# Kernel tuning notes

Measured on AMD Instinct MI355X. Metric: run time of the kernel, lower is better.

Reference implementation:

```python
import jax, jax.numpy as jnp
import numpy as np

N_GRAPHS = 128
N_NODES = 512
N = N_GRAPHS * N_NODES      # 65536 total nodes
E = 524288                  # edges (avg degree 8)
F_IN = 4                    # num_features
EMB = 4                     # embedding_dim
HEADS = 4
GDIM = 16                   # GATConv_dim
D = GDIM * HEADS            # 64 = d_model
NHEAD = 2                   # heads // 2
FF = 64                     # ff_hid_dim
OUT = 64                    # output_dim
N_GAT_REST = 3              # gat_layers - 1


def setup_inputs() -> dict:
    key = jax.random.key(0)
    ks = iter(jax.random.split(key, 64))
    def nrm(shape, fan_in):
        return jax.random.normal(next(ks), shape, jnp.float32) / np.float32(np.sqrt(fan_in))
    inp = {}
    inp['x'] = jax.random.normal(next(ks), (N, F_IN), jnp.float32)
    inp['edge_index'] = jax.random.randint(next(ks), (2, E), 0, N, dtype=jnp.int32)
    inp['batch'] = jnp.repeat(jnp.arange(N_GRAPHS, dtype=jnp.int32), N_NODES)
    # feature_fc
    inp['Wf'] = nrm((F_IN, EMB), F_IN); inp['bf'] = jnp.zeros((EMB,), jnp.float32)
    # input GATConv (EMB -> HEADS*GDIM)
    inp['gW0'] = nrm((EMB, HEADS * GDIM), EMB)
    inp['aS0'] = nrm((HEADS, GDIM), GDIM); inp['aD0'] = nrm((HEADS, GDIM), GDIM)
    inp['gb0'] = jnp.zeros((D,), jnp.float32)
    # remaining 3 GATConv layers (D -> HEADS*GDIM), stacked
    inp['gW'] = nrm((N_GAT_REST, D, HEADS * GDIM), D)
    inp['aS'] = nrm((N_GAT_REST, HEADS, GDIM), GDIM); inp['aD'] = nrm((N_GAT_REST, HEADS, GDIM), GDIM)
    inp['gb'] = jnp.zeros((N_GAT_REST, D), jnp.float32)
    # decoder layer: self-attn, cross-attn, layernorms, FFN
    for p in ['sWq','sWk','sWv','sWo','cWq','cWk','cWv','cWo']:
        inp[p] = nrm((D, D), D)
    for p in ['sbq','sbk','sbv','sbo','cbq','cbk','cbv','cbo']:
        inp[p] = jnp.zeros((D,), jnp.float32)
    for g, b in [('ln1g','ln1b'), ('ln2g','ln2b'), ('ln3g','ln3b')]:
        inp[g] = jnp.ones((D,), jnp.float32); inp[b] = jnp.zeros((D,), jnp.float32)
    inp['ffW1'] = nrm((D, FF), D); inp['ffb1'] = jnp.zeros((FF,), jnp.float32)
    inp['ffW2'] = nrm((FF, D), FF); inp['ffb2'] = jnp.zeros((D,), jnp.float32)
    inp['fcW'] = nrm((D, OUT), D); inp['fcb'] = jnp.zeros((OUT,), jnp.float32)
    return inp


def _gat(h_in, src, dst, W, a_s, a_d, b):
    # PyG GATConv, concat=True, negative_slope=0.2, self-loops already in (src,dst)
    h = (h_in @ W).reshape(N, HEADS, GDIM)
    es = jnp.einsum('nho,ho->nh', h, a_s)   # [N,H]
    ed = jnp.einsum('nho,ho->nh', h, a_d)
    e = jax.nn.leaky_relu(es[src] + ed[dst], 0.2)          # [E',H]
    m = jax.ops.segment_max(e, dst, num_segments=N)        # segment softmax over dst
    w = jnp.exp(e - m[dst])
    s = jax.ops.segment_sum(w, dst, num_segments=N)
    alpha = w / (s[dst] + 1e-16)
    out = jax.ops.segment_sum(h[src] * alpha[..., None], dst, num_segments=N)
    return out.reshape(N, D) + b


def _mha(q, kv, Wq, bq, Wk, bk, Wv, bv, Wo, bo):
    B, S, Dm = q.shape
    hd = Dm // NHEAD
    Q = (q @ Wq + bq).reshape(B, S, NHEAD, hd)
    K = (kv @ Wk + bk).reshape(B, S, NHEAD, hd)
    V = (kv @ Wv + bv).reshape(B, S, NHEAD, hd)
    a = jax.nn.softmax(jnp.einsum('bqhd,bkhd->bhqk', Q, K) / jnp.sqrt(jnp.float32(hd)), axis=-1)
    o = jnp.einsum('bhqk,bkhd->bqhd', a, V).reshape(B, S, Dm)
    return o @ Wo + bo


def _ln(x, g, b):
    m = x.mean(-1, keepdims=True)
    v = ((x - m) ** 2).mean(-1, keepdims=True)
    return (x - m) / jnp.sqrt(v + 1e-5) * g + b


def reference(x, edge_index, batch, Wf, bf, gW0, aS0, aD0, gb0, gW, aS, aD, gb,
              sWq, sWk, sWv, sWo, cWq, cWk, cWv, cWo,
              sbq, sbk, sbv, sbo, cbq, cbk, cbv, cbo,
              ln1g, ln1b, ln2g, ln2b, ln3g, ln3b,
              ffW1, ffb1, ffW2, ffb2, fcW, fcb):
    loops = jnp.arange(N, dtype=edge_index.dtype)
    src = jnp.concatenate([edge_index[0], loops])
    dst = jnp.concatenate([edge_index[1], loops])
    h = x @ Wf + bf
    h = jax.nn.leaky_relu(_gat(h, src, dst, gW0, aS0, aD0, gb0), 0.01)
    for i in range(N_GAT_REST):
        h = jax.nn.leaky_relu(_gat(h, src, dst, gW[i], aS[i], aD[i], gb[i]), 0.01)
    t = h.reshape(N_GRAPHS, N_NODES, D)
    # one transformer decoder layer, post-norm, memory = layer input
    mem = t
    t = _ln(t + _mha(t, t, sWq, sbq, sWk, sbk, sWv, sbv, sWo, sbo), ln1g, ln1b)
    t = _ln(t + _mha(t, mem, cWq, cbq, cWk, cbk, cWv, cbv, cWo, cbo), ln2g, ln2b)
    t = _ln(t + (jax.nn.relu(t @ ffW1 + ffb1) @ ffW2 + ffb2), ln3g, ln3b)
    h = t.reshape(N, D)
    pooled = jax.ops.segment_sum(h, batch, num_segments=N_GRAPHS) / jnp.float32(N_NODES)
    return pooled @ fcW + fcb
```

## Files before the change

### kernel.cpp

```cpp
#include <hip/hip_runtime.h>
#include <math.h>

#define NG 128
#define SEQ 512
#define NN 65536
#define EE 524288
#define DM 64
#define HSTR 80

typedef __attribute__((ext_vector_type(8))) short short8;
typedef __attribute__((ext_vector_type(4))) short short4v;
typedef __attribute__((ext_vector_type(4))) float f32x4;

__device__ __forceinline__ float lrelu(float x, float s){ return x > 0.f ? x : s*x; }

__device__ __forceinline__ unsigned short f2bf(float x){
  union { float f; unsigned u; } v; v.f = x;
  unsigned r = v.u + 0x7FFF + ((v.u>>16)&1);
  return (unsigned short)(r>>16);
}
__device__ __forceinline__ float bf2f(unsigned short x){
  union { unsigned u; float f; } v; v.u = ((unsigned)x)<<16;
  return v.f;
}
// ... 78 lines not shown
    float s = 0.f;
    #pragma unroll
    for (int k=0;k<4;k++) s += Wf[i*4+k]*gW0[k*64+j];
    Wl[i][j] = s;
  }
  if (tid < 64){
    float4 v = *(const float4*)&x[(size_t)(n0+tid)*4];
    inL[0][tid]=v.x; inL[1][tid]=v.y; inL[2][tid]=v.z; inL[3][tid]=v.w;
  }
  __syncthreads();
  int i = tid>>4, j = tid&15;
  float acc[4][4];
  #pragma unroll
  for (int r=0;r<4;r++){
    #pragma unroll
    for (int c=0;c<4;c++) acc[r][c] = 0.f;
  }
  #pragma unroll
  for (int k=0;k<4;k++){
    float4 av = *(float4*)&inL[k][4*i];
    float4 bv = *(float4*)&Wl[k][4*j];
    float a_[4]={av.x,av.y,av.z,av.w}, b_[4]={bv.x,bv.y,bv.z,bv.w};
    #pragma unroll
    for (int r=0;r<4;r++){
      #pragma unroll
      for (int c=0;c<4;c++) acc[r][c] += a_[r]*b_[c];
    }
  }
  float4 asv = *(float4*)&asl[4*j];
  float4 adv = *(float4*)&adl[4*j];
  float4 bbv = *(float4*)&b0l[4*j];
  float bb[4] = {bbv.x, bbv.y, bbv.z, bbv.w};
  #pragma unroll
  for (int r=0;r<4;r++){
    float y0=acc[r][0]+bb[0], y1=acc[r][1]+bb[1], y2=acc[r][2]+bb[2], y3=acc[r][3]+bb[3];
    int node = n0 + 4*i + r;
    ushort4 hv;
    hv.x=f2bf(y0); hv.y=f2bf(y1); hv.z=f2bf(y2); hv.w=f2bf(y3);
    *(ushort4*)&hout[(size_t)node*HSTR + 4*j] = hv;
    float ps = y0*asv.x + y1*asv.y + y2*asv.z + y3*asv.w;
    float pd = y0*adv.x + y1*adv.y + y2*adv.z + y3*adv.w;
    ps += __shfl_xor(ps,1); ps += __shfl_xor(ps,2);
    pd += __shfl_xor(pd,1); pd += __shfl_xor(pd,2);
    if ((j&3)==0){
      *(float*)&hout[(size_t)node*HSTR + 64 + 2*(j>>2)] = ps;
      ed[(size_t)node*4 + (j>>2)] = pd;
    }
  }
}

__global__ void __launch_bounds__(256) k_transform_bf(const unsigned short* __restrict__ hin, const float* __restrict__ W,
                            const float* __restrict__ aSp, const float* __restrict__ aDp,
                            unsigned short* __restrict__ hout, float* __restrict__ ed){
  __shared__ float inL[64][68];
  __shared__ float Wl[64][64];
  __shared__ float asl[64], adl[64];
  int tid = threadIdx.x;
  int n0 = blockIdx.x*64;
  if (tid < 64){ asl[tid] = aSp[tid]; adl[tid] = aDp[tid]; }
  for (int idx=tid; idx<1024; idx+=256){
    int k = idx>>4, jj = (idx&15)<<2;
    *(float4*)&Wl[k][jj] = *(const float4*)&W[k*64+jj];
  }
  for (int idx=tid; idx<1024; idx+=256){
    int node = idx>>4, kk = (idx&15)<<2;
    ushort4 v = *(const ushort4*)&hin[(size_t)(n0+node)*64 + kk];
    inL[kk][node]=bf2f(v.x); inL[kk+1][node]=bf2f(v.y); inL[kk+2][node]=bf2f(v.z); inL[kk+3][node]=bf2f(v.w);
  }
  __syncthreads();
  int i = tid>>4, j = tid&15;
  float acc[4][4];
  #pragma unroll
  for (int r=0;r<4;r++){
    #pragma unroll
    for (int c=0;c<4;c++) acc[r][c] = 0.f;
  }
  #pragma unroll 4
  for (int k=0;k<64;k++){
    float4 av = *(float4*)&inL[k][4*i];
    float4 bv = *(float4*)&Wl[k][4*j];
    float a_[4]={av.x,av.y,av.z,av.w}, b_[4]={bv.x,bv.y,bv.z,bv.w};
    #pragma unroll
    for (int r=0;r<4;r++){
      #pragma unroll
      for (int c=0;c<4;c++) acc[r][c] += a_[r]*b_[c];
    }
  }
  float4 asv = *(float4*)&asl[4*j];
  float4 adv = *(float4*)&adl[4*j];
  #pragma unroll
  for (int r=0;r<4;r++){
    float y0=acc[r][0], y1=acc[r][1], y2=acc[r][2], y3=acc[r][3];
    int node = n0 + 4*i + r;
    ushort4 hv;
    hv.x=f2bf(y0); hv.y=f2bf(y1); hv.z=f2bf(y2); hv.w=f2bf(y3);
    *(ushort4*)&hout[(size_t)node*HSTR + 4*j] = hv;
    float ps = y0*asv.x + y1*asv.y + y2*asv.z + y3*asv.w;
    float pd = y0*adv.x + y1*adv.y + y2*adv.z + y3*adv.w;
    ps += __shfl_xor(ps,1); ps += __shfl_xor(ps,2);
    pd += __shfl_xor(pd,1); pd += __shfl_xor(pd,2);
    if ((j&3)==0){
      *(float*)&hout[(size_t)node*HSTR + 64 + 2*(j>>2)] = ps;
      ed[(size_t)node*4 + (j>>2)] = pd;
    }
  }
}

template<int BF16OUT>
__global__ void __launch_bounds__(256) k_aggregate(const unsigned short* __restrict__ h,
                            const float* __restrict__ ed, const int* __restrict__ rowp,
                            const int* __restrict__ col, const float* __restrict__ gb,
                            void* __restrict__ houtv){
  int tid = threadIdx.x;
  int n = blockIdx.x*4 + (tid>>6);
  int l = tid&63;
  int q = l>>4;
  int sl = l&15;
  int head = sl>>2;
  float edn = ed[(size_t)n*4 + head];
  float es_self = *(const float*)&h[(size_t)n*HSTR + 64 + 2*head];
  int beg = __builtin_amdgcn_readfirstlane(rowp[n]);
  int end = __builtin_amdgcn_readfirstlane(rowp[n+1]);
  float m = -1e30f, s = 0.f;
  float a0=0.f, a1=0.f, a2=0.f, a3=0.f;
  int i = beg;
  for (; i+8 <= end; i += 8){
    int c0=col[i], c1=col[i+1], c2=col[i+2], c3=col[i+3];
    int c4=col[i+4], c5=col[i+5], c6=col[i+6], c7=col[i+7];
    int t01 = (q&1)? c1 : c0;
    int t23 = (q&1)? c3 : c2;
    int sq0 = (q&2)? t23 : t01;
    int t45 = (q&1)? c5 : c4;
    int t67 = (q&1)? c7 : c6;
    int sq1 = (q&2)? t67 : t45;
    size_t b0r = (size_t)sq0*HSTR, b1r = (size_t)sq1*HSTR;
    ushort4 hv0 = *(const ushort4*)&h[b0r + 4*sl];
    ushort4 hv1 = *(const ushort4*)&h[b1r + 4*sl];
    float e0 = lrelu(*(const float*)&h[b0r + 64 + 2*head] + edn, 0.2f);
    float e1 = lrelu(*(const float*)&h[b1r + 64 + 2*head] + edn, 0.2f);
    float mx = fmaxf(e0, e1);
    if (__any(mx > m + 8.f)){
      float nm = fmaxf(m, mx);
      float c = __expf(m - nm);
      s*=c; a0*=c; a1*=c; a2*=c; a3*=c; m = nm;
    }
    float w0 = __expf(e0 - m);
    float w1 = __expf(e1 - m);
    s += w0 + w1;
    a0 += w0*bf2f(hv0.x) + w1*bf2f(hv1.x);
    a1 += w0*bf2f(hv0.y) + w1*bf2f(hv1.y);
    a2 += w0*bf2f(hv0.z) + w1*bf2f(hv1.z);
    a3 += w0*bf2f(hv0.w) + w1*bf2f(hv1.w);
  }
  if (i < end){
    int last = end-1;
    int i1=(i+1<last)?i+1:last, i2=(i+2<last)?i+2:last, i3=(i+3<last)?i+3:last;
    int i4=(i+4<last)?i+4:last, i5=(i+5<last)?i+5:last, i6=(i+6<last)?i+6:last;
    int c0=col[i], c1=col[i1], c2=col[i2], c3=col[i3];
    int c4=col[i4], c5=col[i5], c6=col[i6], c7=col[last];
    int t01 = (q&1)? c1 : c0;
    int t23 = (q&1)? c3 : c2;
    int sq0 = (q&2)? t23 : t01;
    int t45 = (q&1)? c5 : c4;
    int t67 = (q&1)? c7 : c6;
    int sq1 = (q&2)? t67 : t45;
// ... 5 lines not shown
    float e0 = lrelu(*(const float*)&h[b0r + 64 + 2*head] + edn, 0.2f);
    float e1 = lrelu(*(const float*)&h[b1r + 64 + 2*head] + edn, 0.2f);
    if (!ac0) e0 = -1e30f;
    if (!ac1) e1 = -1e30f;
    float mx = fmaxf(e0, e1);
    if (__any(mx > m + 8.f)){
      float nm = fmaxf(m, mx);
      float c = __expf(m - nm);
      s*=c; a0*=c; a1*=c; a2*=c; a3*=c; m = nm;
    }
    float w0 = ac0 ? __expf(e0 - m) : 0.f;
    float w1 = ac1 ? __expf(e1 - m) : 0.f;
    s += w0 + w1;
    a0 += w0*bf2f(hv0.x) + w1*bf2f(hv1.x);
    a1 += w0*bf2f(hv0.y) + w1*bf2f(hv1.y);
    a2 += w0*bf2f(hv0.z) + w1*bf2f(hv1.z);
    a3 += w0*bf2f(hv0.w) + w1*bf2f(hv1.w);
  }
  #pragma unroll
  for (int off=16; off<=32; off<<=1){
    float m2 = __shfl_xor(m, off);
    float s2 = __shfl_xor(s, off);
    float b0 = __shfl_xor(a0, off);
    float b1 = __shfl_xor(a1, off);
    float b2 = __shfl_xor(a2, off);
    float b3 = __shfl_xor(a3, off);
    float nm = fmaxf(m, m2);
    float c1 = __expf(m - nm), c2 = __expf(m2 - nm);
    s  = s*c1  + s2*c2;
    a0 = a0*c1 + b0*c2;
    a1 = a1*c1 + b1*c2;
    a2 = a2*c1 + b2*c2;
    a3 = a3*c1 + b3*c2;
    m = nm;
  }
  {
    float e_self = lrelu(es_self + edn, 0.2f);
    float nm = fmaxf(m, e_self);
    float c = __expf(m - nm), cs = __expf(e_self - nm);
    ushort4 hs = *(const ushort4*)&h[(size_t)n*HSTR + 4*sl];
    s  = s*c  + cs;
    a0 = a0*c + cs*bf2f(hs.x);
    a1 = a1*c + cs*bf2f(hs.y);
    a2 = a2*c + cs*bf2f(hs.z);
    a3 = a3*c + cs*bf2f(hs.w);
  }
  if (q == 0){
    float inv = 1.f/(s + 1e-16f);
    float4 gv = *(const float4*)&gb[4*sl];
    float o0 = lrelu(a0*inv + gv.x, 0.01f);
    float o1 = lrelu(a1*inv + gv.y, 0.01f);
    float o2 = lrelu(a2*inv + gv.z, 0.01f);
    float o3 = lrelu(a3*inv + gv.w, 0.01f);
    if (BF16OUT){
      ushort4 hv; hv.x=f2bf(o0); hv.y=f2bf(o1); hv.z=f2bf(o2); hv.w=f2bf(o3);
      *(ushort4*)((unsigned short*)houtv + (size_t)n*64 + 4*sl) = hv;
    } else {
      *(float4*)((float*)houtv + (size_t)n*64 + 4*sl) = make_float4(o0,o1,o2,o3);
    }
  }
}

__global__ void __launch_bounds__(256) k_qkv3(const float* __restrict__ in0, const float* __restrict__ W0, const float* __restrict__ b0, unsigned short* __restrict__ o0,
                      const float* __restrict__ in1, const float* __restrict__ W1, const float* __restrict__ b1, unsigned short* __restrict__ o1,
                      const float* __restrict__ in2, const float* __restrict__ W2, const float* __restrict__ b2, unsigned short* __restrict__ o2,
                      float scl0){
  __shared__ float inL[64][68];
  __shared__ float Wl[64][64];
  int tid = threadIdx.x;
  int n0 = blockIdx.x*64;
  int i = tid>>4, j = tid&15;
  const float* ins[3] = {in0, in1, in2};
  const float* Ws[3] = {W0, W1, W2};
  const float* bs[3] = {b0, b1, b2};
  unsigned short* os[3] = {o0, o1, o2};
  const float* cur = nullptr;
  for (int w=0; w<3; w++){
    __syncthreads();
    if (ins[w] != cur){
      cur = ins[w];
      for (int idx=tid; idx<1024; idx+=256){
        int node = idx>>4, kk = (idx&15)<<2;
        float4 v = *(const float4*)&cur[(size_t)(n0+node)*64 + kk];
        inL[kk][node]=v.x; inL[kk+1][node]=v.y; inL[kk+2][node]=v.z; inL[kk+3][node]=v.w;
      }
    }
    for (int idx=tid; idx<1024; idx+=256){
      int k = idx>>4, jj = (idx&15)<<2;
      *(float4*)&Wl[k][jj] = *(const float4*)&Ws[w][k*64+jj];
    }
    __syncthreads();
    float acc[4][4];
    #pragma unroll
    for (int r=0;r<4;r++){
      #pragma unroll
      for (int c=0;c<4;c++) acc[r][c] = 0.f;
    }
    #pragma unroll 4
    for (int k=0;k<64;k++){
      float4 av = *(float4*)&inL[k][4*i];
      float4 bv = *(float4*)&Wl[k][4*j];
      float a_[4]={av.x,av.y,av.z,av.w}, b_[4]={bv.x,bv.y,bv.z,bv.w};
      #pragma unroll
      for (int r=0;r<4;r++){
        #pragma unroll
        for (int c=0;c<4;c++) acc[r][c] += a_[r]*b_[c];
      }
    }
    float4 bv = *(const float4*)&bs[w][4*j];
    float bb[4] = {bv.x, bv.y, bv.z, bv.w};
    float sc = (w==0) ? scl0 : 1.f;
    #pragma unroll
    for (int r=0;r<4;r++){
      ushort4 hv;
      hv.x = f2bf((acc[r][0]+bb[0])*sc);
      hv.y = f2bf((acc[r][1]+bb[1])*sc);
      hv.z = f2bf((acc[r][2]+bb[2])*sc);
      hv.w = f2bf((acc[r][3]+bb[3])*sc);
      *(ushort4*)&os[w][(size_t)(n0+4*i+r)*64 + 4*j] = hv;
    }
  }
}

__global__ void __launch_bounds__(256) k_ffn(const float* __restrict__ in,
                     const float* __restrict__ W1p, const float* __restrict__ b1p,
                     const float* __restrict__ W2p, const float* __restrict__ b2p,
                     const float* __restrict__ g, const float* __restrict__ bl,
                     float* __restrict__ out){
  __shared__ float inL[64][68];
  __shared__ float Wl[64][64];
  __shared__ float ffL[64][68];
  int tid = threadIdx.x;
  int n0 = blockIdx.x*64;
  for (int idx=tid; idx<1024; idx+=256){
    int k = idx>>4, jj = (idx&15)<<2;
    *(float4*)&Wl[k][jj] = *(const float4*)&W1p[k*64+jj];
  }
  for (int idx=tid; idx<1024; idx+=256){
    int node = idx>>4, kk = (idx&15)<<2;
    float4 v = *(const float4*)&in[(size_t)(n0+node)*64 + kk];
    inL[kk][node]=v.x; inL[kk+1][node]=v.y; inL[kk+2][node]=v.z; inL[kk+3][node]=v.w;
  }
  __syncthreads();
  int i = tid>>4, j = tid&15;
  float acc[4][4];
  #pragma unroll
  for (int r=0;r<4;r++){
    #pragma unroll
    for (int c=0;c<4;c++) acc[r][c] = 0.f;
  }
  #pragma unroll 4
  for (int k=0;k<64;k++){
    float4 av = *(float4*)&inL[k][4*i];
    float4 bv = *(float4*)&Wl[k][4*j];
    float a_[4]={av.x,av.y,av.z,av.w}, b_[4]={bv.x,bv.y,bv.z,bv.w};
    #pragma unroll
    for (int r=0;r<4;r++){
      #pragma unroll
      for (int c=0;c<4;c++) acc[r][c] += a_[r]*b_[c];
    }
  }
  float4 b1v = *(const float4*)&b1p[4*j];
  float bb1[4] = {b1v.x, b1v.y, b1v.z, b1v.w};
  #pragma unroll
  for (int r=0;r<4;r++){
    #pragma unroll
    for (int c=0;c<4;c++){
      ffL[4*j+c][4*i+r] = fmaxf(acc[r][c] + bb1[c], 0.f);
    }
  }
  __syncthreads();
  for (int idx=tid; idx<1024; idx+=256){
    int k = idx>>4, jj = (idx&15)<<2;
    *(float4*)&Wl[k][jj] = *(const float4*)&W2p[k*64+jj];
  }
  __syncthreads();
  #pragma unroll
  for (int r=0;r<4;r++){
    #pragma unroll
    for (int c=0;c<4;c++) acc[r][c] = 0.f;
  }
  #pragma unroll 4
  for (int k=0;k<64;k++){
    float4 av = *(float4*)&ffL[k][4*i];
    float4 bv = *(float4*)&Wl[k][4*j];
    float a_[4]={av.x,av.y,av.z,av.w}, b_[4]={bv.x,bv.y,bv.z,bv.w};
    #pragma unroll
    for (int r=0;r<4;r++){
      #pragma unroll
      for (int c=0;c<4;c++) acc[r][c] += a_[r]*b_[c];
    }
  }
  float4 b2v = *(const float4*)&b2p[4*j];
  float bb2v[4] = {b2v.x, b2v.y, b2v.z, b2v.w};
  float4 gv = *(const float4*)&g[4*j];
  float4 blv = *(const float4*)&bl[4*j];
  float gg[4] = {gv.x, gv.y, gv.z, gv.w};
  float bbl[4] = {blv.x, blv.y, blv.z, blv.w};
  #pragma unroll
  for (int r=0;r<4;r++){
    int node = n0 + 4*i + r;
    float y[4];
    #pragma unroll
    for (int c=0;c<4;c++) y[c] = acc[r][c] + bb2v[c] + inL[4*j+c][4*i+r];
    float s = (y[0]+y[1]) + (y[2]+y[3]);
    s += __shfl_xor(s,1); s += __shfl_xor(s,2); s += __shfl_xor(s,4); s += __shfl_xor(s,8);
    float mean = s * (1.f/64.f);
    float d[4] = {y[0]-mean, y[1]-mean, y[2]-mean, y[3]-mean};
    float v = (d[0]*d[0]+d[1]*d[1]) + (d[2]*d[2]+d[3]*d[3]);
    v += __shfl_xor(v,1); v += __shfl_xor(v,2); v += __shfl_xor(v,4); v += __shfl_xor(v,8);
    float inv = rsqrtf(v*(1.f/64.f) + 1e-5f);
    *(float4*)&out[(size_t)node*64 + 4*j] =
      make_float4(d[0]*inv*gg[0]+bbl[0], d[1]*inv*gg[1]+bbl[1],
                  d[2]*inv*gg[2]+bbl[2], d[3]*inv*gg[3]+bbl[3]);
  }
}

__global__ void __launch_bounds__(512) k_attn_fused(const unsigned short* __restrict__ Q, const unsigned short* __restrict__ K,
                      const unsigned short* __restrict__ V,
                      const float* __restrict__ Wo, const float* __restrict__ bo,
                      const float* __restrict__ res, const float* __restrict__ g, const float* __restrict__ bl,
                      float* __restrict__ out){
  __shared__ __align__(16) char smem[49152];
  char* Ksm = smem;
  char* Vsm = smem + 16384;
  char* Psm = smem + 32768;

  int bid = blockIdx.x;
  int qq = bid & 3;
  int b  = bid >> 2;
  int tid = threadIdx.x;
  int wave = tid>>6;
  int l = tid & 63;
  int lq = l & 15;
  int g4 = l >> 4;
  int head = wave & 1;
  int qg = wave >> 1;
  const size_t gb = (size_t)b*SEQ*64;
  const int hoff = head*32;
  const f32x4 zero = {0.f,0.f,0.f,0.f};

  int qrow0 = qq*128 + qg*32;
  short8 qf[2];
  f32x4 O[2][2];
  float m_[2], l_[2];
  #pragma unroll
  for (int qt=0; qt<2; qt++){
    qf[qt] = *(const short8*)(Q + gb + (size_t)(qrow0 + qt*16 + lq)*64 + hoff + g4*8);
    O[qt][0] = zero; O[qt][1] = zero;
    m_[qt] = -1e30f; l_[qt] = 0.f;
  }
  char* Pw = Psm + wave*2048;
  int swzp = (lq&7)<<4;
  int d0 = hoff + lq, d1 = hoff + lq + 16;
  int sv0 = (((d0&7) ^ ((d0>>3)&7)) << 4);
  int sv1 = (((d1&7) ^ ((d1>>3)&7)) << 4);

  for (int ph=0; ph<4; ph++){
    __syncthreads();
    #pragma unroll
    for (int it=0; it<2; it++){
      int idx = tid + it*512;
      int row = idx>>3, gr = idx&7;
      uint4 v = *(const uint4*)(K + gb + (size_t)(ph*128 + row)*64 + gr*8);
      *(uint4*)(Ksm + row*128 + ((gr*16) ^ ((row&7)<<4))) = v;
    }
    #pragma unroll
    for (int it=0; it<2; it++){
      int idx = tid + it*512;
      int key = idx>>3, gr = idx&7;
      uint4 vv = *(const uint4*)(V + gb + (size_t)(ph*128 + key)*64 + gr*8);
      const unsigned short* vs = (const unsigned short*)&vv;
      #pragma unroll
      for (int c=0;c<8;c++){
        int d = gr*8 + c;
// ... 73 lines not shown
    lt += __shfl_xor(lt, 32);
    float inv = 1.f/lt;
    int row = qg*32 + qt*16 + lq;
    #pragma unroll
    for (int c=0;c<4;c++){
      OT[(hoff + g4*4 + c)*136 + row]      = f2bf(O[qt][0][c]*inv);
      OT[(hoff + 16 + g4*4 + c)*136 + row] = f2bf(O[qt][1][c]*inv);
    }
  }
  for (int idx=tid; idx<1024; idx+=512){
    int k = idx>>4, jj = (idx&15)<<2;
    *(float4*)&WoL[k*64+jj] = *(const float4*)&Wo[k*64+jj];
  }
  __syncthreads();
  int i = tid>>4, j = tid&15;
  float acc[4][4];
  #pragma unroll
  for (int r=0;r<4;r++){
    #pragma unroll
    for (int c=0;c<4;c++) acc[r][c] = 0.f;
  }
  #pragma unroll 4
  for (int k=0;k<64;k++){
    short4v av = *(short4v*)&OT[k*136 + 4*i];
    float4 bv = *(float4*)&WoL[k*64 + 4*j];
    float b_[4]={bv.x,bv.y,bv.z,bv.w};
    #pragma unroll
    for (int r=0;r<4;r++){
      float a = bf2f((unsigned short)av[r]);
      #pragma unroll
      for (int c=0;c<4;c++) acc[r][c] += a*b_[c];
    }
  }
  float4 bov = *(const float4*)&bo[4*j];
  float4 gv = *(const float4*)&g[4*j];
  float4 blv = *(const float4*)&bl[4*j];
  float bb[4] = {bov.x, bov.y, bov.z, bov.w};
  float gg[4] = {gv.x, gv.y, gv.z, gv.w};
  float bbl[4] = {blv.x, blv.y, blv.z, blv.w};
  #pragma unroll
  for (int r=0;r<4;r++){
    int row = 4*i + r;
    int node = b*SEQ + qq*128 + row;
    float4 rv = *(const float4*)&res[(size_t)node*64 + 4*j];
    float y[4] = {acc[r][0]+bb[0]+rv.x, acc[r][1]+bb[1]+rv.y,
                  acc[r][2]+bb[2]+rv.z, acc[r][3]+bb[3]+rv.w};
    float s = (y[0]+y[1]) + (y[2]+y[3]);
    s += __shfl_xor(s,1); s += __shfl_xor(s,2); s += __shfl_xor(s,4); s += __shfl_xor(s,8);
    float mean = s * (1.f/64.f);
    float d[4] = {y[0]-mean, y[1]-mean, y[2]-mean, y[3]-mean};
    float v = (d[0]*d[0]+d[1]*d[1]) + (d[2]*d[2]+d[3]*d[3]);
    v += __shfl_xor(v,1); v += __shfl_xor(v,2); v += __shfl_xor(v,4); v += __shfl_xor(v,8);
    float inv = rsqrtf(v*(1.f/64.f) + 1e-5f);
    *(float4*)&out[(size_t)node*64 + 4*j] =
      make_float4(d[0]*inv*gg[0]+bbl[0], d[1]*inv*gg[1]+bbl[1],
                  d[2]*inv*gg[2]+bbl[2], d[3]*inv*gg[3]+bbl[3]);
  }
}

__global__ void __launch_bounds__(256) k_pool_fc(const float* __restrict__ t, const float* __restrict__ fcW,
                          const float* __restrict__ fcb, float* __restrict__ out){
  __shared__ float pl[4][64];
  __shared__ float pf[64];
  int b = blockIdx.x;
  int tid = threadIdx.x;
  int j = tid&63, seg = tid>>6;
  const float* basep = t + (size_t)b*SEQ*64;
  float s = 0.f;
  for (int si=seg*128; si<(seg+1)*128; si++) s += basep[(size_t)si*64 + j];
  pl[seg][j] = s;
  __syncthreads();
  if (tid < 64){
    pf[tid] = (pl[0][tid]+pl[1][tid]+pl[2][tid]+pl[3][tid]) * (1.f/512.f);
  }
  __syncthreads();
  if (tid < 64){
    float o = fcb[tid];
    for (int k=0;k<64;k++) o += pf[k]*fcW[k*64+tid];
    out[(size_t)b*64 + tid] = o;
  }
}

extern "C" void kernel_launch(void* const* d_in, const int* in_sizes, int n_in,
                              void* d_out, int out_size, void* d_ws, size_t ws_size,
                              hipStream_t stream) {
  const float* x    = (const float*)d_in[0];
  const int*   ei   = (const int*)d_in[1];
  const float* Wf   = (const float*)d_in[3];
  const float* bf   = (const float*)d_in[4];
  const float* gW0  = (const float*)d_in[5];
  const float* aS0  = (const float*)d_in[6];
  const float* aD0  = (const float*)d_in[7];
  const float* gb0  = (const float*)d_in[8];
  const float* gW   = (const float*)d_in[9];
  const float* aS   = (const float*)d_in[10];
  const float* aD   = (const float*)d_in[11];
  const float* gb   = (const float*)d_in[12];
  const float* sWq  = (const float*)d_in[13];
  const float* sWk  = (const float*)d_in[14];
  const float* sWv  = (const float*)d_in[15];
  const float* sWo  = (const float*)d_in[16];
  const float* cWq  = (const float*)d_in[17];
  const float* cWk  = (const float*)d_in[18];
  const float* cWv  = (const float*)d_in[19];
  const float* cWo  = (const float*)d_in[20];
  const float* sbq  = (const float*)d_in[21];
  const float* sbk  = (const float*)d_in[22];
  const float* sbv  = (const float*)d_in[23];
  const float* sbo  = (const float*)d_in[24];
  const float* cbq  = (const float*)d_in[25];
  const float* cbk  = (const float*)d_in[26];
  const float* cbv  = (const float*)d_in[27];
  const float* cbo  = (const float*)d_in[28];
  const float* ln1g = (const float*)d_in[29];
  const float* ln1b = (const float*)d_in[30];
  const float* ln2g = (const float*)d_in[31];
  const float* ln2b = (const float*)d_in[32];
  const float* ln3g = (const float*)d_in[33];
  const float* ln3b = (const float*)d_in[34];
  const float* ffW1 = (const float*)d_in[35];
  const float* ffb1 = (const float*)d_in[36];
  const float* ffW2 = (const float*)d_in[37];
  const float* ffb2 = (const float*)d_in[38];
  const float* fcW  = (const float*)d_in[39];
  const float* fcb  = (const float*)d_in[40];

  char* ws = (char*)d_ws;
  size_t off = 0;
  auto alloc = [&](size_t bytes) -> void* {
    void* p = ws + off;
    off += (bytes + 255) & ~(size_t)255;
    return p;
  };
  int* deg    = (int*)alloc(NN*sizeof(int));
  int* excl   = (int*)alloc(NN*sizeof(int));
  int* rowp   = (int*)alloc((NN+1)*sizeof(int));
  int* cursor = (int*)alloc(NN*sizeof(int));
  int* col    = (int*)alloc(EE*sizeof(int));
  int* bsums  = (int*)alloc(256*sizeof(int));
  float* ed   = (float*)alloc((size_t)NN*4*sizeof(float));
  unsigned short* Hb   = (unsigned short*)alloc((size_t)NN*HSTR*sizeof(unsigned short));
  unsigned short* Hagg = (unsigned short*)alloc((size_t)NN*64*sizeof(unsigned short));
  unsigned short* Qb = (unsigned short*)alloc((size_t)NN*64*sizeof(unsigned short));
  unsigned short* Kb = (unsigned short*)alloc((size_t)NN*64*sizeof(unsigned short));
  unsigned short* Vb = (unsigned short*)alloc((size_t)NN*64*sizeof(unsigned short));
  float* B1   = (float*)alloc((size_t)NN*64*sizeof(float));
  float* B2   = (float*)alloc((size_t)NN*64*sizeof(float));
  float* B5   = (float*)alloc((size_t)NN*64*sizeof(float));

  const int* e_src = ei;
  const int* e_dst = ei + EE;

  const float scale = 0.17677669529663687f;

  hipMemsetAsync(deg, 0, NN*sizeof(int), stream);
  k_count<<<EE/256, 256, 0, stream>>>(e_dst, deg);
  k_scan1<<<NN/256, 256, 0, stream>>>(deg, excl, bsums);
  k_scan2<<<1, 256, 0, stream>>>(bsums);
  k_scan3<<<NN/256, 256, 0, stream>>>(excl, bsums, rowp, cursor);
  k_fill<<<EE/256, 256, 0, stream>>>(e_src, e_dst, cursor, col);

  k_transform0<<<NN/64, 256, 0, stream>>>(x, Wf, bf, gW0, aS0, aD0, Hb, ed);
  k_aggregate<1><<<NN/4, 256, 0, stream>>>(Hb, ed, rowp, col, gb0, Hagg);
  k_transform_bf<<<NN/64, 256, 0, stream>>>(Hagg, gW+0*4096, aS+0*64, aD+0*64, Hb, ed);
  k_aggregate<1><<<NN/4, 256, 0, stream>>>(Hb, ed, rowp, col, gb+0*64, Hagg);
  k_transform_bf<<<NN/64, 256, 0, stream>>>(Hagg, gW+1*4096, aS+1*64, aD+1*64, Hb, ed);
  k_aggregate<1><<<NN/4, 256, 0, stream>>>(Hb, ed, rowp, col, gb+1*64, Hagg);
  k_transform_bf<<<NN/64, 256, 0, stream>>>(Hagg, gW+2*4096, aS+2*64, aD+2*64, Hb, ed);
  k_aggregate<0><<<NN/4, 256, 0, stream>>>(Hb, ed, rowp, col, gb+2*64, B2);

  k_qkv3<<<NN/64, 256, 0, stream>>>(B2, sWq, sbq, Qb, B2, sWk, sbk, Kb, B2, sWv, sbv, Vb, scale);
  k_attn_fused<<<NG*4, 512, 0, stream>>>(Qb, Kb, Vb, sWo, sbo, B2, ln1g, ln1b, B5);

  k_qkv3<<<NN/64, 256, 0, stream>>>(B5, cWq, cbq, Qb, B2, cWk, cbk, Kb, B2, cWv, cbv, Vb, scale);
  k_attn_fused<<<NG*4, 512, 0, stream>>>(Qb, Kb, Vb, cWo, cbo, B5, ln2g, ln2b, B2);

  k_ffn<<<NN/64, 256, 0, stream>>>(B2, ffW1, ffb1, ffW2, ffb2, ln3g, ln3b, B1);

  k_pool_fc<<<NG, 256, 0, stream>>>(B1, fcW, fcb, (float*)d_out);
}
```

Before: 409.0 us.

## Use bf16 MFMA for dense node transforms, QKV projections and FFN

Replaces the scalar FP32 register-tiled 64x64 GEMMs in the GAT transform, QKV projection and FFN kernels with bf16 MFMA 16x16x32 instructions, staging inputs and transposed weights in swizzled LDS. To feed these, the aggregate and attention kernels now also write bf16 copies of their outputs, so the GEMM kernels read half-width activations. The FP32 residual path is kept for the layernorms. This cuts ALU work and input bandwidth in the GEMM kernels, at the cost of extra bf16 stores and reduced precision in the QKV and FFN inputs.

```diff
diff --git a/kernel.cpp b/kernel.cpp
--- a/kernel.cpp
+++ b/kernel.cpp
@@ -154,65 +154,76 @@
 __global__ void __launch_bounds__(256) k_transform_bf(const unsigned short* __restrict__ hin, const float* __restrict__ W,
                             const float* __restrict__ aSp, const float* __restrict__ aDp,
                             unsigned short* __restrict__ hout, float* __restrict__ ed){
-  __shared__ float inL[64][68];
-  __shared__ float Wl[64][64];
+  __shared__ __align__(16) char Ab[8192];
+  __shared__ __align__(16) char Wt[8192];
   __shared__ float asl[64], adl[64];
   int tid = threadIdx.x;
   int n0 = blockIdx.x*64;
-  if (tid < 64){ asl[tid] = aSp[tid]; adl[tid] = aDp[tid]; }
-  for (int idx=tid; idx<1024; idx+=256){
-    int k = idx>>4, jj = (idx&15)<<2;
-    *(float4*)&Wl[k][jj] = *(const float4*)&W[k*64+jj];
-  }
-  for (int idx=tid; idx<1024; idx+=256){
-    int node = idx>>4, kk = (idx&15)<<2;
-    ushort4 v = *(const ushort4*)&hin[(size_t)(n0+node)*64 + kk];
-    inL[kk][node]=bf2f(v.x); inL[kk+1][node]=bf2f(v.y); inL[kk+2][node]=bf2f(v.z); inL[kk+3][node]=bf2f(v.w);
-  }
-  __syncthreads();
-  int i = tid>>4, j = tid&15;
-  float acc[4][4];
-  #pragma unroll
-  for (int r=0;r<4;r++){
-    #pragma unroll
-    for (int c=0;c<4;c++) acc[r][c] = 0.f;
-  }
-  #pragma unroll 4
-  for (int k=0;k<64;k++){
-    float4 av = *(float4*)&inL[k][4*i];
-    float4 bv = *(float4*)&Wl[k][4*j];
-    float a_[4]={av.x,av.y,av.z,av.w}, b_[4]={bv.x,bv.y,bv.z,bv.w};
+  if (tid < 64){ asl[tid]=aSp[tid]; adl[tid]=aDp[tid]; }
+  #pragma unroll
+  for (int it=0; it<2; it++){
+    int idx = tid + it*256;
+    int row = idx>>3, gr = idx&7;
+    uint4 v = *(const uint4*)(hin + (size_t)(n0+row)*64 + gr*8);
+    *(uint4*)(Ab + row*128 + ((gr*16) ^ ((row&7)<<4))) = v;
+  }
+  #pragma unroll
+  for (int it=0; it<4; it++){
+    int idx = tid + it*256;
+    int k = idx>>4, c4 = (idx&15)<<2;
+    float4 v = *(const float4*)(W + k*64 + c4);
+    float vv[4]={v.x,v.y,v.z,v.w};
+    #pragma unroll
+    for (int c=0;c<4;c++){
+      int col = c4+c;
+      *(unsigned short*)(Wt + col*128 + ((2*k) ^ ((col&7)<<4))) = f2bf(vv[c]);
+    }
+  }
+  __syncthreads();
+  int wave = tid>>6, l=tid&63, lq=l&15, g4=l>>4;
+  int nb = wave*16;
+  const f32x4 zero = {0.f,0.f,0.f,0.f};
+  short8 af[2];
+  #pragma unroll
+  for (int s=0;s<2;s++){
+    int row = nb+lq;
+    af[s] = *(short8*)(Ab + row*128 + (((s*64)+g4*16) ^ ((row&7)<<4)));
+  }
+  f32x4 acc[4];
+  #pragma unroll
+  for (int ct=0;ct<4;ct++){
+    acc[ct]=zero;
+    #pragma unroll
+    for (int s=0;s<2;s++){
+      int col = ct*16+lq;
+      short8 wf = *(short8*)(Wt + col*128 + (((s*64)+g4*16) ^ ((col&7)<<4)));
+      acc[ct] = __builtin_amdgcn_mfma_f32_16x16x32_bf16(af[s], wf, acc[ct], 0,0,0);
+    }
+  }
+  #pragma unroll
+  for (int ct=0;ct<4;ct++){
+    float as_ = asl[ct*16+lq], ad_ = adl[ct*16+lq];
     #pragma unroll
     for (int r=0;r<4;r++){
-      #pragma unroll
-      for (int c=0;c<4;c++) acc[r][c] += a_[r]*b_[c];
-    }
-  }
-  float4 asv = *(float4*)&asl[4*j];
-  float4 adv = *(float4*)&adl[4*j];
-  #pragma unroll
-  for (int r=0;r<4;r++){
-    float y0=acc[r][0], y1=acc[r][1], y2=acc[r][2], y3=acc[r][3];
-    int node = n0 + 4*i + r;
-    ushort4 hv;
-    hv.x=f2bf(y0); hv.y=f2bf(y1); hv.z=f2bf(y2); hv.w=f2bf(y3);
-    *(ushort4*)&hout[(size_t)node*HSTR + 4*j] = hv;
-    float ps = y0*asv.x + y1*asv.y + y2*asv.z + y3*asv.w;
-    float pd = y0*adv.x + y1*adv.y + y2*adv.z + y3*adv.w;
-    ps += __shfl_xor(ps,1); ps += __shfl_xor(ps,2);
-    pd += __shfl_xor(pd,1); pd += __shfl_xor(pd,2);
-    if ((j&3)==0){
-      *(float*)&hout[(size_t)node*HSTR + 64 + 2*(j>>2)] = ps;
-      ed[(size_t)node*4 + (j>>2)] = pd;
-    }
-  }
-}
-
-template<int BF16OUT>
+      float y = acc[ct][r];
+      int node = n0 + nb + 4*g4 + r;
+      hout[(size_t)node*HSTR + ct*16 + lq] = f2bf(y);
+      float ps = y*as_, pd = y*ad_;
+      ps += __shfl_xor(ps,1); ps += __shfl_xor(ps,2); ps += __shfl_xor(ps,4); ps += __shfl_xor(ps,8);
+      pd += __shfl_xor(pd,1); pd += __shfl_xor(pd,2); pd += __shfl_xor(pd,4); pd += __shfl_xor(pd,8);
+      if (lq==0){
+        *(float*)&hout[(size_t)node*HSTR + 64 + 2*ct] = ps;
+        ed[(size_t)node*4 + ct] = pd;
+      }
+    }
+  }
+}
+
+template<int MODE>
 __global__ void __launch_bounds__(256) k_aggregate(const unsigned short* __restrict__ h,
                             const float* __restrict__ ed, const int* __restrict__ rowp,
                             const int* __restrict__ col, const float* __restrict__ gb,
-                            void* __restrict__ houtv){
+                            float* __restrict__ fout, unsigned short* __restrict__ bout){
   int tid = threadIdx.x;
   int n = blockIdx.x*4 + (tid>>6);
   int l = tid&63;
@@ -324,167 +335,196 @@
     float o1 = lrelu(a1*inv + gv.y, 0.01f);
     float o2 = lrelu(a2*inv + gv.z, 0.01f);
     float o3 = lrelu(a3*inv + gv.w, 0.01f);
-    if (BF16OUT){
+    if (MODE==0 || MODE==2){
+      *(float4*)(fout + (size_t)n*64 + 4*sl) = make_float4(o0,o1,o2,o3);
+    }
+    if (MODE==1 || MODE==2){
       ushort4 hv; hv.x=f2bf(o0); hv.y=f2bf(o1); hv.z=f2bf(o2); hv.w=f2bf(o3);
-      *(ushort4*)((unsigned short*)houtv + (size_t)n*64 + 4*sl) = hv;
-    } else {
-      *(float4*)((float*)houtv + (size_t)n*64 + 4*sl) = make_float4(o0,o1,o2,o3);
-    }
-  }
-}
-
-__global__ void __launch_bounds__(256) k_qkv3(const float* __restrict__ in0, const float* __restrict__ W0, const float* __restrict__ b0, unsigned short* __restrict__ o0,
-                      const float* __restrict__ in1, const float* __restrict__ W1, const float* __restrict__ b1, unsigned short* __restrict__ o1,
-                      const float* __restrict__ in2, const float* __restrict__ W2, const float* __restrict__ b2, unsigned short* __restrict__ o2,
+      *(ushort4*)(bout + (size_t)n*64 + 4*sl) = hv;
+    }
+  }
+}
+
+__global__ void __launch_bounds__(256) k_qkv3(const unsigned short* __restrict__ in0, const float* __restrict__ W0, const float* __restrict__ b0, unsigned short* __restrict__ o0,
+                      const unsigned short* __restrict__ in1, const float* __restrict__ W1, const float* __restrict__ b1, unsigned short* __restrict__ o1,
+                      const unsigned short* __restrict__ in2, const float* __restrict__ W2, const float* __restrict__ b2, unsigned short* __restrict__ o2,
                       float scl0){
-  __shared__ float inL[64][68];
-  __shared__ float Wl[64][64];
+  __shared__ __align__(16) char Ab[8192];
+  __shared__ __align__(16) char Wt[8192];
   int tid = threadIdx.x;
   int n0 = blockIdx.x*64;
-  int i = tid>>4, j = tid&15;
-  const float* ins[3] = {in0, in1, in2};
+  int wave = tid>>6, l=tid&63, lq=l&15, g4=l>>4;
+  int nb = wave*16;
+  const f32x4 zero = {0.f,0.f,0.f,0.f};
+  const unsigned short* ins[3] = {in0, in1, in2};
   const float* Ws[3] = {W0, W1, W2};
   const float* bs[3] = {b0, b1, b2};
   unsigned short* os[3] = {o0, o1, o2};
-  const float* cur = nullptr;
+  const unsigned short* cur = nullptr;
+  short8 af[2];
   for (int w=0; w<3; w++){
+    bool restage = (ins[w] != cur);
     __syncthreads();
-    if (ins[w] != cur){
+    if (restage){
       cur = ins[w];
-      for (int idx=tid; idx<1024; idx+=256){
-        int node = idx>>4, kk = (idx&15)<<2;
-        float4 v = *(const float4*)&cur[(size_t)(n0+node)*64 + kk];
-        inL[kk][node]=v.x; inL[kk+1][node]=v.y; inL[kk+2][node]=v.z; inL[kk+3][node]=v.w;
+      #pragma unroll
+      for (int it=0; it<2; it++){
+        int idx = tid + it*256;
+        int row = idx>>3, gr = idx&7;
+        uint4 v = *(const uint4*)(cur + (size_t)(n0+row)*64 + gr*8);
+        *(uint4*)(Ab + row*128 + ((gr*16) ^ ((row&7)<<4))) = v;
       }
     }
-    for (int idx=tid; idx<1024; idx+=256){
-      int k = idx>>4, jj = (idx&15)<<2;
-      *(float4*)&Wl[k][jj] = *(const float4*)&Ws[w][k*64+jj];
+    #pragma unroll
+    for (int it=0; it<4; it++){
+      int idx = tid + it*256;
+      int k = idx>>4, c4 = (idx&15)<<2;
+      float4 v = *(const float4*)(Ws[w] + k*64 + c4);
+      float vv[4]={v.x,v.y,v.z,v.w};
+      #pragma unroll
+      for (int c=0;c<4;c++){
+        int colc = c4+c;
+        *(unsigned short*)(Wt + colc*128 + ((2*k) ^ ((colc&7)<<4))) = f2bf(vv[c]);
+      }
     }
     __syncthreads();
-    float acc[4][4];
-    #pragma unroll
-    for (int r=0;r<4;r++){
+    if (restage){
       #pragma unroll
-      for (int c=0;c<4;c++) acc[r][c] = 0.f;
-    }
-    #pragma unroll 4
-    for (int k=0;k<64;k++){
-      float4 av = *(float4*)&inL[k][4*i];
-      float4 bv = *(float4*)&Wl[k][4*j];
-      float a_[4]={av.x,av.y,av.z,av.w}, b_[4]={bv.x,bv.y,bv.z,bv.w};
+      for (int s=0;s<2;s++){
+        int row = nb+lq;
+        af[s] = *(short8*)(Ab + row*128 + (((s*64)+g4*16) ^ ((row&7)<<4)));
+      }
+    }
+    float sc = (w==0) ? scl0 : 1.f;
+    #pragma unroll
+    for (int ct=0;ct<4;ct++){
+      f32x4 acc = zero;
+      #pragma unroll
+      for (int s=0;s<2;s++){
+        int colc = ct*16+lq;
+        short8 wf = *(short8*)(Wt + colc*128 + (((s*64)+g4*16) ^ ((colc&7)<<4)));
+        acc = __builtin_amdgcn_mfma_f32_16x16x32_bf16(af[s], wf, acc, 0,0,0);
+      }
+      float bv = bs[w][ct*16+lq];
       #pragma unroll
       for (int r=0;r<4;r++){
-        #pragma unroll
-        for (int c=0;c<4;c++) acc[r][c] += a_[r]*b_[c];
+        int node = n0 + nb + 4*g4 + r;
+        os[w][(size_t)node*64 + ct*16 + lq] = f2bf((acc[r] + bv)*sc);
       }
     }
-    float4 bv = *(const float4*)&bs[w][4*j];
-    float bb[4] = {bv.x, bv.y, bv.z, bv.w};
-    float sc = (w==0) ? scl0 : 1.f;
-    #pragma unroll
-    for (int r=0;r<4;r++){
-      ushort4 hv;
-      hv.x = f2bf((acc[r][0]+bb[0])*sc);
-      hv.y = f2bf((acc[r][1]+bb[1])*sc);
-      hv.z = f2bf((acc[r][2]+bb[2])*sc);
-      hv.w = f2bf((acc[r][3]+bb[3])*sc);
-      *(ushort4*)&os[w][(size_t)(n0+4*i+r)*64 + 4*j] = hv;
-    }
-  }
-}
-
-__global__ void __launch_bounds__(256) k_ffn(const float* __restrict__ in,
+  }
+}
+
+__global__ void __launch_bounds__(256) k_ffn(const unsigned short* __restrict__ inb, const float* __restrict__ inf,
                      const float* __restrict__ W1p, const float* __restrict__ b1p,
                      const float* __restrict__ W2p, const float* __restrict__ b2p,
                      const float* __restrict__ g, const float* __restrict__ bl,
                      float* __restrict__ out){
-  __shared__ float inL[64][68];
-  __shared__ float Wl[64][64];
-  __shared__ float ffL[64][68];
+  __shared__ __align__(16) char Ab[8192];
+  __shared__ __align__(16) char Wt[8192];
   int tid = threadIdx.x;
   int n0 = blockIdx.x*64;
-  for (int idx=tid; idx<1024; idx+=256){
-    int k = idx>>4, jj = (idx&15)<<2;
-    *(float4*)&Wl[k][jj] = *(const float4*)&W1p[k*64+jj];
-  }
-  for (int idx=tid; idx<1024; idx+=256){
-    int node = idx>>4, kk = (idx&15)<<2;
-    float4 v = *(const float4*)&in[(size_t)(n0+node)*64 + kk];
-    inL[kk][node]=v.x; inL[kk+1][node]=v.y; inL[kk+2][node]=v.z; inL[kk+3][node]=v.w;
-  }
-  __syncthreads();
-  int i = tid>>4, j = tid&15;
-  float acc[4][4];
+  int wave = tid>>6, l=tid&63, lq=l&15, g4=l>>4;
+  int nb = wave*16;
+  const f32x4 zero = {0.f,0.f,0.f,0.f};
+  #pragma unroll
+  for (int it=0; it<2; it++){
+    int idx = tid + it*256;
+    int row = idx>>3, gr = idx&7;
+    uint4 v = *(const uint4*)(inb + (size_t)(n0+row)*64 + gr*8);
+    *(uint4*)(Ab + row*128 + ((gr*16) ^ ((row&7)<<4))) = v;
+  }
+  #pragma unroll
+  for (int it=0; it<4; it++){
+    int idx = tid + it*256;
+    int k = idx>>4, c4 = (idx&15)<<2;
+    float4 v = *(const float4*)(W1p + k*64 + c4);
+    float vv[4]={v.x,v.y,v.z,v.w};
+    #pragma unroll
+    for (int c=0;c<4;c++){
+      int colc = c4+c;
+      *(unsigned short*)(Wt + colc*128 + ((2*k) ^ ((colc&7)<<4))) = f2bf(vv[c]);
+    }
+  }
+  __syncthreads();
+  short8 af[2];
+  #pragma unroll
+  for (int s=0;s<2;s++){
+    int row = nb+lq;
+    af[s] = *(short8*)(Ab + row*128 + (((s*64)+g4*16) ^ ((row&7)<<4)));
+  }
+  #pragma unroll
+  for (int ct=0;ct<4;ct++){
+    f32x4 acc = zero;
+    #pragma unroll
+    for (int s=0;s<2;s++){
+      int colc = ct*16+lq;
+      short8 wf = *(short8*)(Wt + colc*128 + (((s*64)+g4*16) ^ ((colc&7)<<4)));
+      acc = __builtin_amdgcn_mfma_f32_16x16x32_bf16(af[s], wf, acc, 0,0,0);
+    }
+    float bv = b1p[ct*16+lq];
+    #pragma unroll
+    for (int r=0;r<4;r++){
+      int row = nb + 4*g4 + r;
+      float y = fmaxf(acc[r] + bv, 0.f);
+      *(unsigned short*)(Ab + row*128 + ((2*(ct*16+lq)) ^ ((row&7)<<4))) = f2bf(y);
+    }
+  }
+  __syncthreads();
+  #pragma unroll
+  for (int it=0; it<4; it++){
+    int idx = tid + it*256;
+    int k = idx>>4, c4 = (idx&15)<<2;
+    float4 v = *(const float4*)(W2p + k*64 + c4);
+    float vv[4]={v.x,v.y,v.z,v.w};
+    #pragma unroll
+    for (int c=0;c<4;c++){
+      int colc = c4+c;
+      *(unsigned short*)(Wt + colc*128 + ((2*k) ^ ((colc&7)<<4))) = f2bf(vv[c]);
+    }
+  }
+  __syncthreads();
+  #pragma unroll
+  for (int s=0;s<2;s++){
+    int row = nb+lq;
+    af[s] = *(short8*)(Ab + row*128 + (((s*64)+g4*16) ^ ((row&7)<<4)));
+  }
+  float yv[4][4];
+  #pragma unroll
+  for (int ct=0;ct<4;ct++){
+    f32x4 acc = zero;
+    #pragma unroll
+    for (int s=0;s<2;s++){
+      int colc = ct*16+lq;
+      short8 wf = *(short8*)(Wt + colc*128 + (((s*64)+g4*16) ^ ((colc&7)<<4)));
+      acc = __builtin_amdgcn_mfma_f32_16x16x32_bf16(af[s], wf, acc, 0,0,0);
+    }
+    float bv = b2p[ct*16+lq];
+    #pragma unroll
+    for (int r=0;r<4;r++){
+      int node = n0 + nb + 4*g4 + r;
+      yv[ct][r] = acc[r] + bv + inf[(size_t)node*64 + ct*16 + lq];
+    }
+  }
+  float gg[4], bbl[4];
+  #pragma unroll
+  for (int ct=0;ct<4;ct++){ gg[ct]=g[ct*16+lq]; bbl[ct]=bl[ct*16+lq]; }
   #pragma unroll
   for (int r=0;r<4;r++){
-    #pragma unroll
-    for (int c=0;c<4;c++) acc[r][c] = 0.f;
-  }
-  #pragma unroll 4
-  for (int k=0;k<64;k++){
-    float4 av = *(float4*)&inL[k][4*i];
-    float4 bv = *(float4*)&Wl[k][4*j];
-    float a_[4]={av.x,av.y,av.z,av.w}, b_[4]={bv.x,bv.y,bv.z,bv.w};
-    #pragma unroll
-    for (int r=0;r<4;r++){
-      #pragma unroll
-      for (int c=0;c<4;c++) acc[r][c] += a_[r]*b_[c];
-    }
-  }
-  float4 b1v = *(const float4*)&b1p[4*j];
-  float bb1[4] = {b1v.x, b1v.y, b1v.z, b1v.w};
-  #pragma unroll
-  for (int r=0;r<4;r++){
-    #pragma unroll
-    for (int c=0;c<4;c++){
-      ffL[4*j+c][4*i+r] = fmaxf(acc[r][c] + bb1[c], 0.f);
-    }
-  }
-  __syncthreads();
-  for (int idx=tid; idx<1024; idx+=256){
-    int k = idx>>4, jj = (idx&15)<<2;
-    *(float4*)&Wl[k][jj] = *(const float4*)&W2p[k*64+jj];
-  }
-  __syncthreads();
-  #pragma unroll
-  for (int r=0;r<4;r++){
-    #pragma unroll
-    for (int c=0;c<4;c++) acc[r][c] = 0.f;
-  }
-  #pragma unroll 4
-  for (int k=0;k<64;k++){
-    float4 av = *(float4*)&ffL[k][4*i];
-    float4 bv = *(float4*)&Wl[k][4*j];
-    float a_[4]={av.x,av.y,av.z,av.w}, b_[4]={bv.x,bv.y,bv.z,bv.w};
-    #pragma unroll
-    for (int r=0;r<4;r++){
-      #pragma unroll
-      for (int c=0;c<4;c++) acc[r][c] += a_[r]*b_[c];
-    }
-  }
-  float4 b2v = *(const float4*)&b2p[4*j];
-  float bb2v[4] = {b2v.x, b2v.y, b2v.z, b2v.w};
-  float4 gv = *(const float4*)&g[4*j];
-  float4 blv = *(const float4*)&bl[4*j];
-  float gg[4] = {gv.x, gv.y, gv.z, gv.w};
-  float bbl[4] = {blv.x, blv.y, blv.z, blv.w};
-  #pragma unroll
-  for (int r=0;r<4;r++){
-    int node = n0 + 4*i + r;
-    float y[4];
-    #pragma unroll
-    for (int c=0;c<4;c++) y[c] = acc[r][c] + bb2v[c] + inL[4*j+c][4*i+r];
-    float s = (y[0]+y[1]) + (y[2]+y[3]);
+    int node = n0 + nb + 4*g4 + r;
+    float s = (yv[0][r]+yv[1][r]) + (yv[2][r]+yv[3][r]);
     s += __shfl_xor(s,1); s += __shfl_xor(s,2); s += __shfl_xor(s,4); s += __shfl_xor(s,8);
     float mean = s * (1.f/64.f);
-    float d[4] = {y[0]-mean, y[1]-mean, y[2]-mean, y[3]-mean};
+    float d[4];
+    #pragma unroll
+    for (int ct=0;ct<4;ct++) d[ct] = yv[ct][r] - mean;
     float v = (d[0]*d[0]+d[1]*d[1]) + (d[2]*d[2]+d[3]*d[3]);
     v += __shfl_xor(v,1); v += __shfl_xor(v,2); v += __shfl_xor(v,4); v += __shfl_xor(v,8);
     float inv = rsqrtf(v*(1.f/64.f) + 1e-5f);
-    *(float4*)&out[(size_t)node*64 + 4*j] =
-      make_float4(d[0]*inv*gg[0]+bbl[0], d[1]*inv*gg[1]+bbl[1],
-                  d[2]*inv*gg[2]+bbl[2], d[3]*inv*gg[3]+bbl[3]);
+    #pragma unroll
+    for (int ct=0;ct<4;ct++){
+      out[(size_t)node*64 + ct*16 + lq] = d[ct]*inv*gg[ct] + bbl[ct];
+    }
   }
 }
 
@@ -492,7 +532,7 @@
                       const unsigned short* __restrict__ V,
                       const float* __restrict__ Wo, const float* __restrict__ bo,
                       const float* __restrict__ res, const float* __restrict__ g, const float* __restrict__ bl,
-                      float* __restrict__ out){
+                      float* __restrict__ out, unsigned short* __restrict__ outb){
   __shared__ __align__(16) char smem[49152];
   char* Ksm = smem;
   char* Vsm = smem + 16384;
@@ -672,9 +712,13 @@
     float v = (d[0]*d[0]+d[1]*d[1]) + (d[2]*d[2]+d[3]*d[3]);
     v += __shfl_xor(v,1); v += __shfl_xor(v,2); v += __shfl_xor(v,4); v += __shfl_xor(v,8);
     float inv = rsqrtf(v*(1.f/64.f) + 1e-5f);
-    *(float4*)&out[(size_t)node*64 + 4*j] =
-      make_float4(d[0]*inv*gg[0]+bbl[0], d[1]*inv*gg[1]+bbl[1],
-                  d[2]*inv*gg[2]+bbl[2], d[3]*inv*gg[3]+bbl[3]);
+    float o0 = d[0]*inv*gg[0]+bbl[0];
+    float o1 = d[1]*inv*gg[1]+bbl[1];
+    float o2 = d[2]*inv*gg[2]+bbl[2];
+    float o3 = d[3]*inv*gg[3]+bbl[3];
+    *(float4*)&out[(size_t)node*64 + 4*j] = make_float4(o0,o1,o2,o3);
+    ushort4 ob; ob.x=f2bf(o0); ob.y=f2bf(o1); ob.z=f2bf(o2); ob.w=f2bf(o3);
+    *(ushort4*)&outb[(size_t)node*64 + 4*j] = ob;
   }
 }
 
@@ -761,9 +805,11 @@
   float* ed   = (float*)alloc((size_t)NN*4*sizeof(float));
   unsigned short* Hb   = (unsigned short*)alloc((size_t)NN*HSTR*sizeof(unsigned short));
   unsigned short* Hagg = (unsigned short*)alloc((size_t)NN*64*sizeof(unsigned short));
-  unsigned short* Qb = (unsigned short*)alloc((size_t)NN*64*sizeof(unsigned short));
-  unsigned short* Kb = (unsigned short*)alloc((size_t)NN*64*sizeof(unsigned short));
-  unsigned short* Vb = (unsigned short*)alloc((size_t)NN*64*sizeof(unsigned short));
+  unsigned short* Qb  = (unsigned short*)alloc((size_t)NN*64*sizeof(unsigned short));
+  unsigned short* Kb  = (unsigned short*)alloc((size_t)NN*64*sizeof(unsigned short));
+  unsigned short* Vb  = (unsigned short*)alloc((size_t)NN*64*sizeof(unsigned short));
+  unsigned short* B5b = (unsigned short*)alloc((size_t)NN*64*sizeof(unsigned short));
+  unsigned short* B2b = (unsigned short*)alloc((size_t)NN*64*sizeof(unsigned short));
   float* B1   = (float*)alloc((size_t)NN*64*sizeof(float));
   float* B2   = (float*)alloc((size_t)NN*64*sizeof(float));
   float* B5   = (float*)alloc((size_t)NN*64*sizeof(float));
@@ -781,21 +827,21 @@
   k_fill<<<EE/256, 256, 0, stream>>>(e_src, e_dst, cursor, col);
 
   k_transform0<<<NN/64, 256, 0, stream>>>(x, Wf, bf, gW0, aS0, aD0, Hb, ed);
-  k_aggregate<1><<<NN/4, 256, 0, stream>>>(Hb, ed, rowp, col, gb0, Hagg);
+  k_aggregate<1><<<NN/4, 256, 0, stream>>>(Hb, ed, rowp, col, gb0, nullptr, Hagg);
   k_transform_bf<<<NN/64, 256, 0, stream>>>(Hagg, gW+0*4096, aS+0*64, aD+0*64, Hb, ed);
-  k_aggregate<1><<<NN/4, 256, 0, stream>>>(Hb, ed, rowp, col, gb+0*64, Hagg);
+  k_aggregate<1><<<NN/4, 256, 0, stream>>>(Hb, ed, rowp, col, gb+0*64, nullptr, Hagg);
   k_transform_bf<<<NN/64, 256, 0, stream>>>(Hagg, gW+1*4096, aS+1*64, aD+1*64, Hb, ed);
-  k_aggregate<1><<<NN/4, 256, 0, stream>>>(Hb, ed, rowp, col, gb+1*64, Hagg);
+  k_aggregate<1><<<NN/4, 256, 0, stream>>>(Hb, ed, rowp, col, gb+1*64, nullptr, Hagg);
   k_transform_bf<<<NN/64, 256, 0, stream>>>(Hagg, gW+2*4096, aS+2*64, aD+2*64, Hb, ed);
-  k_aggregate<0><<<NN/4, 256, 0, stream>>>(Hb, ed, rowp, col, gb+2*64, B2);
-
-  k_qkv3<<<NN/64, 256, 0, stream>>>(B2, sWq, sbq, Qb, B2, sWk, sbk, Kb, B2, sWv, sbv, Vb, scale);
-  k_attn_fused<<<NG*4, 512, 0, stream>>>(Qb, Kb, Vb, sWo, sbo, B2, ln1g, ln1b, B5);
-
-  k_qkv3<<<NN/64, 256, 0, stream>>>(B5, cWq, cbq, Qb, B2, cWk, cbk, Kb, B2, cWv, cbv, Vb, scale);
-  k_attn_fused<<<NG*4, 512, 0, stream>>>(Qb, Kb, Vb, cWo, cbo, B5, ln2g, ln2b, B2);
-
-  k_ffn<<<NN/64, 256, 0, stream>>>(B2, ffW1, ffb1, ffW2, ffb2, ln3g, ln3b, B1);
+  k_aggregate<2><<<NN/4, 256, 0, stream>>>(Hb, ed, rowp, col, gb+2*64, B2, Hagg);
+
+  k_qkv3<<<NN/64, 256, 0, stream>>>(Hagg, sWq, sbq, Qb, Hagg, sWk, sbk, Kb, Hagg, sWv, sbv, Vb, scale);
+  k_attn_fused<<<NG*4, 512, 0, stream>>>(Qb, Kb, Vb, sWo, sbo, B2, ln1g, ln1b, B5, B5b);
+
+  k_qkv3<<<NN/64, 256, 0, stream>>>(B5b, cWq, cbq, Qb, Hagg, cWk, cbk, Kb, Hagg, cWv, cbv, Vb, scale);
+  k_attn_fused<<<NG*4, 512, 0, stream>>>(Qb, Kb, Vb, cWo, cbo, B5, ln2g, ln2b, B2, B2b);
+
+  k_ffn<<<NN/64, 256, 0, stream>>>(B2b, B2, ffW1, ffb1, ffW2, ffb2, ln3g, ln3b, B1);
 
   k_pool_fc<<<NG, 256, 0, stream>>>(B1, fcW, fcb, (float*)d_out);
 }
```

After: 368.0 us (median of 2 runs). -10.0%, faster.
